# Kernel optimization log

Measured on AMD Instinct MI355X. Metric: run time of the kernel, lower is better.

Reference implementation:

```python
import jax, jax.numpy as jnp
import numpy as np

H = 1024       # hidden_dim
NH = 16        # num_attention_heads
HD = H // NH   # head_dim = 64
ROT = 32       # rotary_dim
MP = 8         # MP_NUM hardcoded in forward
NEG_INF = jnp.float32(-1e9)


def setup_inputs() -> dict:
    key = jax.random.key(0)
    k1, k2, k3 = jax.random.split(key, 3)
    hidden_states = jax.random.normal(k1, (2, 2048, H), dtype=jnp.float32)
    w_qkv = jax.random.normal(k2, (H, 3 * H), dtype=jnp.float32) * 0.02
    w_out = jax.random.normal(k3, (H, H), dtype=jnp.float32) * 0.02
    return {"hidden_states": hidden_states, "w_qkv": w_qkv, "w_out": w_out}


def _rotate_every_two(x):
    # GPT-J rotate: (x0,x1,x2,x3,...) -> (-x1,x0,-x3,x2,...)
    x1 = x[..., ::2]
    x2 = x[..., 1::2]
    return jnp.stack((-x2, x1), axis=-1).reshape(x.shape)


def _apply_rope(x, sin, cos):
    return x * cos + _rotate_every_two(x) * sin


def reference(hidden_states, w_qkv, w_out):
    B, S, _ = hidden_states.shape
    qkv = hidden_states @ w_qkv                      # [B,S,3H]
    qkv = qkv.reshape(B, S, MP, 3 * H // MP)         # GPT-J MP-split layout
    local = NH * HD // MP
    q = qkv[..., :local]
    k = qkv[..., local:2 * local]
    v = qkv[..., 2 * local:]

    def split_heads(x):  # [B,S,MP,H/MP] -> [B,S,NH,HD]
        return x.reshape(B, S, MP, NH // MP, HD).reshape(B, S, NH, HD)

    q, k, v = split_heads(q), split_heads(k), split_heads(v)

    # fixed position embedding (GPT-J), offset=0, seq dim = 1
    inv_freq = 1.0 / (10000.0 ** (jnp.arange(0, ROT, 2, dtype=jnp.float32) / ROT))
    sinusoid = jnp.einsum('i,j->ij', jnp.arange(S, dtype=jnp.float32), inv_freq)  # [S,ROT/2]
    sin = jnp.repeat(jnp.sin(sinusoid), 2, axis=-1)[None, :, None, :]             # [1,S,1,ROT]
    cos = jnp.repeat(jnp.cos(sinusoid), 2, axis=-1)[None, :, None, :]

    q = jnp.concatenate([_apply_rope(q[..., :ROT], sin, cos), q[..., ROT:]], axis=-1)
    k = jnp.concatenate([_apply_rope(k[..., :ROT], sin, cos), k[..., ROT:]], axis=-1)

    q = q.transpose(0, 2, 1, 3)  # [B,NH,S,HD]
    k = k.transpose(0, 2, 1, 3)
    v = v.transpose(0, 2, 1, 3)

    # manual causal attention in fp32 (as the torch code casts q,k to fp32)
    scores = jnp.einsum('bhqd,bhkd->bhqk', q, k) / jnp.sqrt(jnp.float32(HD))
    causal = jnp.tril(jnp.ones((S, S), dtype=bool))[None, None]
    scores = jnp.where(causal, scores, NEG_INF)
    probs = jax.nn.softmax(scores, axis=-1)
    attn = jnp.einsum('bhqk,bhkd->bhqd', probs, v)   # [B,NH,S,HD]

    attn = attn.transpose(0, 2, 1, 3).reshape(B, S, H)  # merge heads
    return attn @ w_out
```

## Files before the change

### kernel.cpp

```cpp
#include <hip/hip_runtime.h>

#define SEQ   2048
#define NHEADS 16
#define HDIM  64
#define HID   1024
#define ROT   32

typedef __attribute__((ext_vector_type(8))) short  short8;
typedef __attribute__((ext_vector_type(4))) float  floatx4;

__device__ __forceinline__ ushort f2bf(float f) {
    union { float f; uint u; } v; v.f = f;
    uint x = v.u;
    uint r = (x + 0x7FFFu + ((x >> 16) & 1u)) >> 16;
    return (ushort)r;
}

__device__ __forceinline__ float fexp2(float x) {
    return __builtin_amdgcn_exp2f(x);
}

__device__ __forceinline__ floatx4 mfma_bf16(short8 a, short8 b, floatx4 c) {
    return __builtin_amdgcn_mfma_f32_16x16x32_bf16(a, b, c, 0, 0, 0);
}

__device__ __forceinline__ void gload16(const ushort* g, ushort* l) {
    __builtin_amdgcn_global_load_lds(
        (const __attribute__((address_space(1))) void*)g,
        (__attribute__((address_space(3))) void*)l, 16, 0, 0);
}

__global__ __launch_bounds__(256) void convert_bf16_kernel(
    const float* __restrict__ src, ushort* __restrict__ dst, int n)
{
    int i = (blockIdx.x * 256 + threadIdx.x) * 8;
    if (i >= n) return;
    float4 a = *(const float4*)(src + i);
    float4 b = *(const float4*)(src + i + 4);
    short8 v;
    v[0] = (short)f2bf(a.x); v[1] = (short)f2bf(a.y);
    v[2] = (short)f2bf(a.z); v[3] = (short)f2bf(a.w);
    v[4] = (short)f2bf(b.x); v[5] = (short)f2bf(b.y);
    v[6] = (short)f2bf(b.z); v[7] = (short)f2bf(b.w);
    *(short8*)(dst + i) = v;
}

__global__ __launch_bounds__(256) void transpose_bf16_kernel(
    const float* __restrict__ src, ushort* __restrict__ dst, int K, int N)
{
    __shared__ ushort Tl[64 * 68];
    const int k0 = blockIdx.y * 64, n0 = blockIdx.x * 64;
    const int tid = threadIdx.x;
    #pragma unroll
    for (int i = 0; i < 4; i++) {
        int lin = tid + 256 * i;
        int row = lin >> 4;
        int c4  = (lin & 15) * 4;
        float4 v = *(const float4*)(src + (size_t)(k0 + row) * N + n0 + c4);
        uint2 u;
        u.x = (uint)f2bf(v.x) | ((uint)f2bf(v.y) << 16);
        u.y = (uint)f2bf(v.z) | ((uint)f2bf(v.w) << 16);
        *(uint2*)&Tl[row * 68 + c4] = u;
    }
    __syncthreads();
    #pragma unroll
    for (int j = 0; j < 2; j++) {
        int lin = tid + 256 * j;
        int n = lin >> 3, c = lin & 7;
        short8 v;
        #pragma unroll
        for (int u = 0; u < 8; u++) v[u] = (short)Tl[(c * 8 + u) * 68 + n];
        *(short8*)(dst + (size_t)(n0 + n) * K + k0 + c * 8) = v;
    }
}

__global__ __launch_bounds__(512) void qkv_rope_kernel(
    const ushort* __restrict__ hbf,
    const ushort* __restrict__ wqkvT,
    ushort* __restrict__ Qb, ushort* __restrict__ Kb, ushort* __restrict__ Vb)
{
    __shared__ ushort Al[3 * 4096];
    __shared__ ushort Bl[3 * 8192];
    const int tid  = threadIdx.x;
    const int lane = tid & 63;
    const int wv   = tid >> 6;
    const int g    = lane >> 4;
    const int l15  = lane & 15;

    const int lin  = blockIdx.x + 12 * blockIdx.y;
    const int xcd  = lin & 7;
    const int slot = lin >> 3;
    const int cxi  = xcd & 1, cyi = xcd >> 1;
    const int sx   = slot % 6, sy = slot / 6;
    const int n0   = (cxi * 6 + sx) * 256;
    const int m0   = (cyi * 8 + sy) * 128;

    const int wr = (wv >> 2) * 64;
    const int wc = (wv & 3) * 64;

    floatx4 acc[4][4];
    #pragma unroll
    for (int a = 0; a < 4; a++)
        #pragma unroll
        for (int bq = 0; bq < 4; bq++)
            acc[a][bq] = floatx4{0.f, 0.f, 0.f, 0.f};

    const int gsw = ((tid & 3) ^ ((tid >> 3) & 3)) * 8;
    const ushort* ga  = hbf   + (size_t)(m0 + (tid >> 2)) * 1024 + gsw;
    const ushort* gb0 = wqkvT + (size_t)(n0 + (tid >> 2)) * 1024 + gsw;
    const ushort* gb1 = gb0 + (size_t)128 * 1024;
    const int wofs = wv * 512;

    auto stage = [&](int t, int ao, int bo) {
        const int k0 = t * 32;
        gload16(ga  + k0, &Al[ao + wofs]);
        gload16(gb0 + k0, &Bl[bo + wofs]);
        gload16(gb1 + k0, &Bl[bo + 4096 + wofs]);
    };

    int a0 = 0, a1 = 4096, a2 = 8192;
    int b0 = 0, b1 = 8192, b2 = 16384;
    stage(0, a0, b0);
    stage(1, a1, b1);
    asm volatile("s_waitcnt vmcnt(3)" ::: "memory");
    __builtin_amdgcn_s_barrier();

    for (int it = 0; it < 32; it++) {
        const bool pre = (it + 2 < 32);
        if (pre) stage(it + 2, a2, b2);
        short8 af[4], bfr[4];
        #pragma unroll
        for (int fm = 0; fm < 4; fm++) {
            const int ra = wr + fm * 16 + l15;
            af[fm] = *(const short8*)&Al[a0 + ((ra * 32 + g * 8) ^ (((ra >> 1) & 3) << 3))];
        }
        #pragma unroll
        for (int fn = 0; fn < 4; fn++) {
            const int rb = wc + fn * 16 + l15;
            bfr[fn] = *(const short8*)&Bl[b0 + ((rb * 32 + g * 8) ^ (((rb >> 1) & 3) << 3))];
        }
        #pragma unroll
        for (int fm = 0; fm < 4; fm++)
            #pragma unroll
            for (int fn = 0; fn < 4; fn++)
                acc[fm][fn] = mfma_bf16(af[fm], bfr[fn], acc[fm][fn]);
        if (pre) asm volatile("s_waitcnt vmcnt(3)" ::: "memory");
        else     asm volatile("s_waitcnt vmcnt(0)" ::: "memory");
        __builtin_amdgcn_s_barrier();
        int t0 = a0; a0 = a1; a1 = a2; a2 = t0;
        int t1 = b0; b0 = b1; b1 = b2; b2 = t1;
    }

    #pragma unroll
    for (int fn = 0; fn < 4; fn++) {
        const int c    = n0 + wc + fn * 16 + l15;
        const int mp   = c / 384;
        const int rem  = c - mp * 384;
        const int tsel = rem >> 7;
        const int j    = (rem >> 6) & 1;
        const int d    = rem & 63;
        const int head = mp * 2 + j;
        ushort* basep = (tsel == 0) ? Qb : (tsel == 1) ? Kb : Vb;
        const bool rope = (tsel < 2) && (d < ROT);
        const float qscale = (tsel == 0) ? 0.18033688011112042f : 1.0f;
        float freq = 0.f;
        if (rope) {
            freq = exp2f((float)(d >> 1) * -0.830482023721841f);
        }
        #pragma unroll
        for (int fm = 0; fm < 4; fm++) {
            #pragma unroll
            for (int r = 0; r < 4; r++) {
                int row = m0 + wr + fm * 16 + g * 4 + r;
                int bb  = row >> 11;
                int s   = row & 2047;
                float val = acc[fm][fn][r];
                float pv  = __shfl_xor(val, 1, 64);
                float outv = val;
                if (rope) {
                    float ang = (float)s * freq;
                    float sn, cs;
                    __sincosf(ang, &sn, &cs);
                    outv = ((d & 1) == 0) ? (val * cs - pv * sn)
                                          : (val * cs + pv * sn);
                }
                outv *= qscale;
                size_t off;
                if (tsel == 2)
                    off = ((size_t)(bb * NHEADS + head) * HDIM + d) * SEQ + s;
                else
                    off = ((size_t)(bb * NHEADS + head) * SEQ + s) * HDIM + d;
                basep[off] = f2bf(outv);
            }
        }
    }
}

__global__ __launch_bounds__(512, 4) void attn_kernel(
    const ushort* __restrict__ Qb, const ushort* __restrict__ Kb,
    const ushort* __restrict__ Vb, ushort* __restrict__ attn)
{
    __shared__ ushort Kl[2][64 * 72];
    __shared__ ushort Vt[2][64 * 72];

    const int tid  = threadIdx.x;
    const int lane = tid & 63;
    const int wv   = tid >> 6;
    const int g    = lane >> 4;
    const int l15  = lane & 15;

    const int l    = blockIdx.x + 16 * blockIdx.y + 256 * blockIdx.z;
    const int half = l >> 8;
    const int xx   = l & 15;
    const int hh   = (l >> 4) & 15;
    const int qb   = half ? xx : 15 - xx;
    const int bb   = half;

    const int q0 = qb * 128;
    const int wq = wv * 16;
    const size_t kvbase = (size_t)(bb * NHEADS + hh) * SEQ * HDIM;

    const int srow = tid >> 3;
    const int sch  = (tid & 7) * 8;

    short8 qreg[2];
    #pragma unroll
    for (int ks = 0; ks < 2; ks++)
        qreg[ks] = *(const short8*)(Qb + kvbase +
            (size_t)(q0 + wq + l15) * HDIM + ks * 32 + g * 8);

    float m = -__builtin_inff();
    float lsum = 0.f;
    floatx4 of[4];
    #pragma unroll
    for (int df = 0; df < 4; df++) of[df] = floatx4{0.f, 0.f, 0.f, 0.f};

    const int nt = 2 * qb + 2;

    auto load_tile = [&](int tt, short8& kr, short8& vr) {
        const int kv = tt * 64;
        kr = *(const short8*)(Kb + kvbase + (size_t)(kv + srow) * HDIM + sch);
        vr = *(const short8*)(Vb + kvbase + (size_t)srow * SEQ + kv + sch);
    };
    auto write_tile = [&](int buf, short8& kr, short8& vr) {
        *(short8*)&Kl[buf][srow * 72 + sch] = kr;
        *(short8*)&Vt[buf][srow * 72 + sch] = vr;
    };
    auto compute_tile = [&](int t, const ushort* Kc, const ushort* Vc) {
        const int kv0 = t * 64;
        if (kv0 > q0 + wq + 15) return;
        floatx4 sf[4];
        __builtin_amdgcn_s_setprio(1);
        #pragma unroll
        for (int kf = 0; kf < 4; kf++) {
            short8 kr0 = *(const short8*)&Kc[(kf * 16 + l15) * 72 + g * 8];
            short8 kr1 = *(const short8*)&Kc[(kf * 16 + l15) * 72 + 32 + g * 8];
            floatx4 s = floatx4{0.f, 0.f, 0.f, 0.f};
            s = mfma_bf16(kr0, qreg[0], s);
            s = mfma_bf16(kr1, qreg[1], s);
            sf[kf] = s;
        }
        __builtin_amdgcn_s_setprio(0);

        const bool diag = (kv0 + 63 > q0 + wq);
        const int qg = q0 + wq + l15;
        float tmax = -__builtin_inff();
        if (diag) {
            #pragma unroll
            for (int kf = 0; kf < 4; kf++) {
                #pragma unroll
                for (int r = 0; r < 4; r++) {
                    int key = kv0 + kf * 16 + g * 4 + r;
                    float x = sf[kf][r];
                    if (key > qg) x = -1e9f;
                    sf[kf][r] = x;
                    tmax = fmaxf(tmax, x);
                }
            }
        } else {
            #pragma unroll
            for (int kf = 0; kf < 4; kf++)
                #pragma unroll
                for (int r = 0; r < 4; r++)
                    tmax = fmaxf(tmax, sf[kf][r]);
        }
        if (!__all(tmax <= m + 8.0f)) {
            tmax = fmaxf(tmax, __shfl_xor(tmax, 16, 64));
            tmax = fmaxf(tmax, __shfl_xor(tmax, 32, 64));
            float mn = fmaxf(m, tmax);
            float f  = fexp2(m - mn);
            m = mn;
            lsum *= f;
            #pragma unroll
            for (int r = 0; r < 4; r++) {
                float fr = __shfl(f, g * 4 + r, 64);
                #pragma unroll
                for (int df = 0; df < 4; df++)
                    of[df][r] *= fr;
            }
        }
        float rs = 0.f;
        #pragma unroll
        for (int kf = 0; kf < 4; kf++) {
            #pragma unroll
            for (int r = 0; r < 4; r++) {
                float p = fexp2(sf[kf][r] - m);
                sf[kf][r] = p;
                rs += p;
            }
        }
        lsum += rs;
        short8 pa[2];
        #pragma unroll
        for (int ks = 0; ks < 2; ks++) {
            union { short8 s; uint u[4]; } pu;
            #pragma unroll
            for (int w = 0; w < 4; w++) {
                const int kf = 2 * ks + (w >> 1);
                float lo = sf[kf][(w & 1) * 2 + 0];
                float hi = sf[kf][(w & 1) * 2 + 1];
                asm("v_cvt_pk_bf16_f32 %0, %1, %2"
                    : "=v"(pu.u[w]) : "v"(lo), "v"(hi));
            }
            pa[ks] = pu.s;
        }
        __builtin_amdgcn_s_setprio(1);
        #pragma unroll
        for (int df = 0; df < 4; df++) {
            #pragma unroll
            for (int ks = 0; ks < 2; ks++) {
                const int vb = (df * 16 + l15) * 72 + ks * 32 + g * 4;
                uint2 v0 = *(const uint2*)&Vc[vb];
                uint2 v1 = *(const uint2*)&Vc[vb + 16];
                union { short8 s; uint4 u; } vv;
                vv.u.x = v0.x; vv.u.y = v0.y; vv.u.z = v1.x; vv.u.w = v1.y;
                of[df] = mfma_bf16(pa[ks], vv.s, of[df]);
            }
        }
        __builtin_amdgcn_s_setprio(0);
    };

    short8 kA, vA, kB, vB;
    load_tile(0, kA, vA);
    if (nt > 1) load_tile(1, kB, vB);
    write_tile(0, kA, vA);
    __syncthreads();

    for (int t = 0; t < nt; t += 2) {
        if (t + 2 < nt) load_tile(t + 2, kA, vA);
        compute_tile(t, Kl[0], Vt[0]);
        write_tile(1, kB, vB);
        __syncthreads();
        if (t + 3 < nt) load_tile(t + 3, kB, vB);
        compute_tile(t + 1, Kl[1], Vt[1]);
        if (t + 2 < nt) write_tile(0, kA, vA);
        __syncthreads();
    }

    lsum += __shfl_xor(lsum, 16, 64);
    lsum += __shfl_xor(lsum, 32, 64);
    #pragma unroll
    for (int r = 0; r < 4; r++) {
        float lr = __shfl(lsum, g * 4 + r, 64);
        float inv = 1.0f / lr;
        int q = q0 + wq + g * 4 + r;
        #pragma unroll
        for (int df = 0; df < 4; df++)
            attn[((size_t)bb * SEQ + q) * HID + hh * 64 + df * 16 + l15] =
                f2bf(of[df][r] * inv);
    }
}

__global__ __launch_bounds__(256) void out_proj_kernel(
    const ushort* __restrict__ attn,
    const ushort* __restrict__ woutT,
    float* __restrict__ out)
{
    __shared__ ushort Al[3 * 4096];
    __shared__ ushort Bl[3 * 4096];
    const int tid  = threadIdx.x;
    const int lane = tid & 63;
    const int wv   = tid >> 6;
    const int g    = lane >> 4;
    const int l15  = lane & 15;

    const int lin  = blockIdx.x + 8 * blockIdx.y;
    const int xcd  = lin & 7;
    const int slot = lin >> 3;
    const int cxi  = xcd & 1, cyi = xcd >> 1;
    const int sx   = slot & 3, sy = slot >> 2;
    const int n0   = (cxi * 4 + sx) * 128;
    const int m0   = (cyi * 8 + sy) * 128;

    const int wr = (wv >> 1) * 64;
    const int wc = (wv & 1) * 64;
    const int rowl = lane >> 2;
    const int kcol = ((lane & 3) ^ ((lane >> 3) & 3)) * 8;

    floatx4 acc[4][4];
    #pragma unroll
    for (int a = 0; a < 4; a++)
        #pragma unroll
        for (int bq = 0; bq < 4; bq++)
            acc[a][bq] = floatx4{0.f, 0.f, 0.f, 0.f};

    const ushort* ga = attn  + (size_t)(m0 + wv * 32 + rowl) * 1024 + kcol;
    const ushort* gb = woutT + (size_t)(n0 + wv * 32 + rowl) * 1024 + kcol;
    const int lofs = wv * 1024;

    auto stage = [&](int t, int ao, int bo) {
        const int k0 = t * 32;
        gload16(ga + k0,             &Al[ao + lofs]);
        gload16(ga + k0 + 16 * 1024, &Al[ao + lofs + 512]);
        gload16(gb + k0,             &Bl[bo + lofs]);
        gload16(gb + k0 + 16 * 1024, &Bl[bo + lofs + 512]);
    };

    int a0 = 0, a1 = 4096, a2 = 8192;
    int b0 = 0, b1 = 4096, b2 = 8192;
    stage(0, a0, b0);
    stage(1, a1, b1);
    asm volatile("s_waitcnt vmcnt(4)" ::: "memory");
    __builtin_amdgcn_s_barrier();

    for (int it = 0; it < 32; it++) {
        const bool pre = (it + 2 < 32);
        if (pre) stage(it + 2, a2, b2);
        short8 af[4], bfr[4];
        #pragma unroll
        for (int fm = 0; fm < 4; fm++) {
            const int ra = wr + fm * 16 + l15;
            af[fm] = *(const short8*)&Al[a0 + ((ra * 32 + g * 8) ^ (((ra >> 1) & 3) << 3))];
        }
        #pragma unroll
        for (int fn = 0; fn < 4; fn++) {
            const int rb = wc + fn * 16 + l15;
            bfr[fn] = *(const short8*)&Bl[b0 + ((rb * 32 + g * 8) ^ (((rb >> 1) & 3) << 3))];
        }
        #pragma unroll
        for (int fm = 0; fm < 4; fm++)
            #pragma unroll
            for (int fn = 0; fn < 4; fn++)
                acc[fm][fn] = mfma_bf16(af[fm], bfr[fn], acc[fm][fn]);
        if (pre) asm volatile("s_waitcnt vmcnt(4)" ::: "memory");
        else     asm volatile("s_waitcnt vmcnt(0)" ::: "memory");
        __builtin_amdgcn_s_barrier();
        int t0 = a0; a0 = a1; a1 = a2; a2 = t0;
        int t1 = b0; b0 = b1; b1 = b2; b2 = t1;
    }
    #pragma unroll
    for (int fm = 0; fm < 4; fm++)
        #pragma unroll
        for (int fn = 0; fn < 4; fn++)
            #pragma unroll
            for (int r = 0; r < 4; r++) {
                int row = m0 + wr + fm * 16 + g * 4 + r;
                int col = n0 + wc + fn * 16 + l15;
                out[(size_t)row * 1024 + col] = acc[fm][fn][r];
            }
}

extern "C" void kernel_launch(void* const* d_in, const int* in_sizes, int n_in,
                              void* d_out, int out_size, void* d_ws, size_t ws_size,
                              hipStream_t stream)
{
    const float* hidden = (const float*)d_in[0];
    const float* wqkv   = (const float*)d_in[1];
    const float* wout   = (const float*)d_in[2];
    float* out = (float*)d_out;

    const size_t NELEM = (size_t)2 * SEQ * HID;
    ushort* Qb    = (ushort*)d_ws;
    ushort* Kb    = Qb + NELEM;
    ushort* Vb    = Kb + NELEM;
    ushort* hbf   = Vb + NELEM;
    ushort* wqkvT = hbf + NELEM;
    ushort* woutT = wqkvT + (size_t)3072 * 1024;
    ushort* attnb = hbf;

    convert_bf16_kernel<<<2048, 256, 0, stream>>>(hidden, hbf, (int)NELEM);
    transpose_bf16_kernel<<<dim3(48, 16), 256, 0, stream>>>(wqkv, wqkvT, 1024, 3072);
    transpose_bf16_kernel<<<dim3(16, 16), 256, 0, stream>>>(wout, woutT, 1024, 1024);
    qkv_rope_kernel<<<dim3(12, 32), 512, 0, stream>>>(hbf, wqkvT, Qb, Kb, Vb);
    attn_kernel<<<dim3(16, NHEADS, 2), 512, 0, stream>>>(Qb, Kb, Vb, attnb);
    out_proj_kernel<<<dim3(8, 32), 256, 0, stream>>>(attnb, woutT, out);
}
```

Measured before the change: 126.7 us.

## Merge prep kernels into one launch and stage attention K/V via direct LDS loads

The bf16 convert and the two weight-transpose kernels become a single prepass kernel that dispatches on block index, removing two launches and the gaps between them. The attention kernel stops staging K/V through registers with padded LDS rows. It now uses global_load_lds straight into XOR-swizzled 64-wide LDS tiles, with one tile per iteration double-buffered. This cuts register pressure and LDS footprint, but it adds a vmcnt wait and a barrier on every tile and depends on the swizzle indexing being correct.

Result: no change. 126.1 us (-0.5%).

```diff
diff --git a/kernel.cpp b/kernel.cpp
--- a/kernel.cpp
+++ b/kernel.cpp
@@ -30,27 +30,10 @@
         (__attribute__((address_space(3))) void*)l, 16, 0, 0);
 }
 
-__global__ __launch_bounds__(256) void convert_bf16_kernel(
-    const float* __restrict__ src, ushort* __restrict__ dst, int n)
-{
-    int i = (blockIdx.x * 256 + threadIdx.x) * 8;
-    if (i >= n) return;
-    float4 a = *(const float4*)(src + i);
-    float4 b = *(const float4*)(src + i + 4);
-    short8 v;
-    v[0] = (short)f2bf(a.x); v[1] = (short)f2bf(a.y);
-    v[2] = (short)f2bf(a.z); v[3] = (short)f2bf(a.w);
-    v[4] = (short)f2bf(b.x); v[5] = (short)f2bf(b.y);
-    v[6] = (short)f2bf(b.z); v[7] = (short)f2bf(b.w);
-    *(short8*)(dst + i) = v;
-}
-
-__global__ __launch_bounds__(256) void transpose_bf16_kernel(
-    const float* __restrict__ src, ushort* __restrict__ dst, int K, int N)
-{
-    __shared__ ushort Tl[64 * 68];
-    const int k0 = blockIdx.y * 64, n0 = blockIdx.x * 64;
-    const int tid = threadIdx.x;
+__device__ __forceinline__ void transpose_tile(
+    const float* __restrict__ src, ushort* __restrict__ dst,
+    int K, int N, int k0, int n0, int tid, ushort* Tl)
+{
     #pragma unroll
     for (int i = 0; i < 4; i++) {
         int lin = tid + 256 * i;
@@ -71,6 +54,35 @@
         #pragma unroll
         for (int u = 0; u < 8; u++) v[u] = (short)Tl[(c * 8 + u) * 68 + n];
         *(short8*)(dst + (size_t)(n0 + n) * K + k0 + c * 8) = v;
+    }
+}
+
+__global__ __launch_bounds__(256) void prepass_kernel(
+    const float* __restrict__ hidden, const float* __restrict__ wqkv,
+    const float* __restrict__ wout, ushort* __restrict__ hbf,
+    ushort* __restrict__ wqkvT, ushort* __restrict__ woutT)
+{
+    __shared__ ushort Tl[64 * 68];
+    const int bid = blockIdx.x;
+    const int tid = threadIdx.x;
+    if (bid < 2048) {
+        int i = (bid * 256 + tid) * 8;
+        float4 a = *(const float4*)(hidden + i);
+        float4 b = *(const float4*)(hidden + i + 4);
+        short8 v;
+        v[0] = (short)f2bf(a.x); v[1] = (short)f2bf(a.y);
+        v[2] = (short)f2bf(a.z); v[3] = (short)f2bf(a.w);
+        v[4] = (short)f2bf(b.x); v[5] = (short)f2bf(b.y);
+        v[6] = (short)f2bf(b.z); v[7] = (short)f2bf(b.w);
+        *(short8*)(hbf + i) = v;
+    } else if (bid < 2048 + 768) {
+        const int lin = bid - 2048;
+        transpose_tile(wqkv, wqkvT, 1024, 3072,
+                       (lin / 48) * 64, (lin % 48) * 64, tid, Tl);
+    } else {
+        const int lin = bid - 2816;
+        transpose_tile(wout, woutT, 1024, 1024,
+                       (lin / 16) * 64, (lin % 16) * 64, tid, Tl);
     }
 }
 
@@ -200,8 +212,8 @@
     const ushort* __restrict__ Qb, const ushort* __restrict__ Kb,
     const ushort* __restrict__ Vb, ushort* __restrict__ attn)
 {
-    __shared__ ushort Kl[2][64 * 72];
-    __shared__ ushort Vt[2][64 * 72];
+    __shared__ ushort Kl[2][64 * 64];
+    __shared__ ushort Vt[2][64 * 64];
 
     const int tid  = threadIdx.x;
     const int lane = tid & 63;
@@ -221,7 +233,8 @@
     const size_t kvbase = (size_t)(bb * NHEADS + hh) * SEQ * HDIM;
 
     const int srow = tid >> 3;
-    const int sch  = (tid & 7) * 8;
+    const int scsw = ((tid & 7) ^ (srow & 7)) * 8;
+    const int wofs = wv * 512;
 
     short8 qreg[2];
     #pragma unroll
@@ -237,15 +250,12 @@
 
     const int nt = 2 * qb + 2;
 
-    auto load_tile = [&](int tt, short8& kr, short8& vr) {
+    auto stage = [&](int tt, int buf) {
         const int kv = tt * 64;
-        kr = *(const short8*)(Kb + kvbase + (size_t)(kv + srow) * HDIM + sch);
-        vr = *(const short8*)(Vb + kvbase + (size_t)srow * SEQ + kv + sch);
+        gload16(Kb + kvbase + (size_t)(kv + srow) * HDIM + scsw, &Kl[buf][wofs]);
+        gload16(Vb + kvbase + (size_t)srow * SEQ + kv + scsw,   &Vt[buf][wofs]);
     };
-    auto write_tile = [&](int buf, short8& kr, short8& vr) {
-        *(short8*)&Kl[buf][srow * 72 + sch] = kr;
-        *(short8*)&Vt[buf][srow * 72 + sch] = vr;
-    };
+
     auto compute_tile = [&](int t, const ushort* Kc, const ushort* Vc) {
         const int kv0 = t * 64;
         if (kv0 > q0 + wq + 15) return;
@@ -253,8 +263,11 @@
         __builtin_amdgcn_s_setprio(1);
         #pragma unroll
         for (int kf = 0; kf < 4; kf++) {
-            short8 kr0 = *(const short8*)&Kc[(kf * 16 + l15) * 72 + g * 8];
-            short8 kr1 = *(const short8*)&Kc[(kf * 16 + l15) * 72 + 32 + g * 8];
+            const int key = kf * 16 + l15;
+            const int rb  = key * 64;
+            const int sw  = key & 7;
+            short8 kr0 = *(const short8*)&Kc[rb + ((g ^ sw) << 3)];
+            short8 kr1 = *(const short8*)&Kc[rb + (((g + 4) ^ sw) << 3)];
             floatx4 s = floatx4{0.f, 0.f, 0.f, 0.f};
             s = mfma_bf16(kr0, qreg[0], s);
             s = mfma_bf16(kr1, qreg[1], s);
@@ -327,11 +340,14 @@
         __builtin_amdgcn_s_setprio(1);
         #pragma unroll
         for (int df = 0; df < 4; df++) {
+            const int d  = df * 16 + l15;
+            const int rb = d * 64;
+            const int sw = d & 7;
             #pragma unroll
             for (int ks = 0; ks < 2; ks++) {
-                const int vb = (df * 16 + l15) * 72 + ks * 32 + g * 4;
-                uint2 v0 = *(const uint2*)&Vc[vb];
-                uint2 v1 = *(const uint2*)&Vc[vb + 16];
+                const int c0 = ks * 4 + (g >> 1);
+                uint2 v0 = *(const uint2*)&Vc[rb + ((c0 ^ sw) << 3) + (g & 1) * 4];
+                uint2 v1 = *(const uint2*)&Vc[rb + (((c0 + 2) ^ sw) << 3) + (g & 1) * 4];
                 union { short8 s; uint4 u; } vv;
                 vv.u.x = v0.x; vv.u.y = v0.y; vv.u.z = v1.x; vv.u.w = v1.y;
                 of[df] = mfma_bf16(pa[ks], vv.s, of[df]);
@@ -340,21 +356,17 @@
         __builtin_amdgcn_s_setprio(0);
     };
 
-    short8 kA, vA, kB, vB;
-    load_tile(0, kA, vA);
-    if (nt > 1) load_tile(1, kB, vB);
-    write_tile(0, kA, vA);
-    __syncthreads();
-
-    for (int t = 0; t < nt; t += 2) {
-        if (t + 2 < nt) load_tile(t + 2, kA, vA);
-        compute_tile(t, Kl[0], Vt[0]);
-        write_tile(1, kB, vB);
-        __syncthreads();
-        if (t + 3 < nt) load_tile(t + 3, kB, vB);
-        compute_tile(t + 1, Kl[1], Vt[1]);
-        if (t + 2 < nt) write_tile(0, kA, vA);
-        __syncthreads();
+    stage(0, 0);
+    asm volatile("s_waitcnt vmcnt(0)" ::: "memory");
+    __builtin_amdgcn_s_barrier();
+
+    int cur = 0;
+    for (int t = 0; t < nt; t++) {
+        if (t + 1 < nt) stage(t + 1, cur ^ 1);
+        compute_tile(t, Kl[cur], Vt[cur]);
+        asm volatile("s_waitcnt vmcnt(0)" ::: "memory");
+        __builtin_amdgcn_s_barrier();
+        cur ^= 1;
     }
 
     lsum += __shfl_xor(lsum, 16, 64);
@@ -478,9 +490,7 @@
     ushort* woutT = wqkvT + (size_t)3072 * 1024;
     ushort* attnb = hbf;
 
-    convert_bf16_kernel<<<2048, 256, 0, stream>>>(hidden, hbf, (int)NELEM);
-    transpose_bf16_kernel<<<dim3(48, 16), 256, 0, stream>>>(wqkv, wqkvT, 1024, 3072);
-    transpose_bf16_kernel<<<dim3(16, 16), 256, 0, stream>>>(wout, woutT, 1024, 1024);
+    prepass_kernel<<<3072, 256, 0, stream>>>(hidden, wqkv, wout, hbf, wqkvT, woutT);
     qkv_rope_kernel<<<dim3(12, 32), 512, 0, stream>>>(hbf, wqkvT, Qb, Kb, Vb);
     attn_kernel<<<dim3(16, NHEADS, 2), 512, 0, stream>>>(Qb, Kb, Vb, attnb);
     out_proj_kernel<<<dim3(8, 32), 256, 0, stream>>>(attnb, woutT, out);
```
